# Kernel tuning notes

Hardware: AMD Instinct MI355X
Metric: run time of the kernel (lower is better)

## Reference

```python
import jax, jax.numpy as jnp
import numpy as np

B, T, DIM, LDIM, NAUX = 4096, 64, 16, 64, 32
H, AH = 256, 128
DT = 0.01
N_SHIFTS = 64
EPS = 1e-5


def _bn(x, g, b):
    # BatchNorm1d in training mode: batch stats, biased variance
    m = jnp.mean(x, 0)
    v = jnp.mean((x - m) ** 2, 0)
    return (x - m) / jnp.sqrt(v + EPS) * g + b


def _forward(xs, enc_bn_gamma, enc_bn_beta, enc_W1, enc_b1, enc_W2, enc_b2, enc_W3,
             enc_scale, aux_bn_gamma, aux_bn_beta, aux_W1, aux_b1, aux_W2, aux_b2,
             aux_W3, aux_scale, Cw):
    lrelu = jax.nn.leaky_relu  # negative_slope=0.01, matches F.leaky_relu default

    # ---- aux nets: 32 small MLPs on x0, vectorized over net index k ----
    x0 = xs[:, 0, :]                                   # [B, DIM]
    m = jnp.mean(x0, 0)
    v = jnp.mean((x0 - m) ** 2, 0)
    xn = (x0 - m) / jnp.sqrt(v + EPS)                  # shared batch stats
    xa = xn[None] * aux_bn_gamma[:, None, :] + aux_bn_beta[:, None, :]  # [K,B,DIM]
    h = lrelu(jnp.einsum('kbi,kji->kbj', xa, aux_W1) + aux_b1[:, None, :])
    h = lrelu(jnp.einsum('kbi,kji->kbj', h, aux_W2) + aux_b2[:, None, :])
    aux = (jnp.einsum('kbi,kji->kbj', h, aux_W3) * aux_scale[:, None, :])
    aux = aux.transpose(1, 0, 2)                       # [B, NAUX, 2] = (mu, omega)

    scale = jnp.exp(aux[..., 0] * DT)                  # [B, NAUX]
    cost = jnp.cos(aux[..., 1] * DT) * scale
    sint = jnp.sin(aux[..., 1] * DT) * scale

    # ---- encoder over trajectory ----
    xs_t = xs[:, :N_SHIFTS, :]                         # [B, T, DIM]
    xf = _bn(xs_t.reshape(-1, DIM), enc_bn_gamma, enc_bn_beta)
    hf = lrelu(xf @ enc_W1.T + enc_b1)
    hf = lrelu(hf @ enc_W2.T + enc_b2)
    yenc = ((hf @ enc_W3.T) * enc_scale).reshape(B, N_SHIFTS, LDIM)
    y = jnp.concatenate((xs_t, yenc), -1)              # [B, T, DIM+LDIM]

    # ---- Jordan-block Koopman recurrence: y @ blockdiag([[c,s],[-s,c]]) ----
    y0 = yenc[:, 0]                                    # [B, LDIM]

    def step(yc, _):
        yb = yc.reshape(B, NAUX, 2)
        o0 = cost * yb[..., 0] - sint * yb[..., 1]
        o1 = sint * yb[..., 0] + cost * yb[..., 1]
        yn = jnp.stack((o0, o1), -1).reshape(B, LDIM)
        return yn, (yn @ Cw.T, yn)

    _, (xseq, yseq) = jax.lax.scan(step, y0, None, length=N_SHIFTS - 1)
    x_pred = jnp.concatenate((xs_t[:, :1], xseq.transpose(1, 0, 2)), 1)   # [B,T,DIM]
    yl_pred = jnp.concatenate((y0[:, None], yseq.transpose(1, 0, 2)), 1)  # [B,T,LDIM]
    y_pred = jnp.concatenate((x_pred, yl_pred), -1)
    return y, y_pred


def setup_inputs() -> dict:
    key = jax.random.key(0)
    ks = jax.random.split(key, 10)
    r = lambda k, s, sc: jax.random.normal(k, s, jnp.float32) * sc
    return {
        'xs': jax.random.normal(ks[0], (B, T, DIM), jnp.float32),
        'enc_bn_gamma': jnp.ones((DIM,), jnp.float32),
        'enc_bn_beta': jnp.zeros((DIM,), jnp.float32),
        'enc_W1': r(ks[1], (H, DIM), 0.2),
        'enc_b1': jnp.zeros((H,), jnp.float32),
        'enc_W2': r(ks[2], (H, H), 0.06),
        'enc_b2': jnp.zeros((H,), jnp.float32),
        'enc_W3': r(ks[3], (LDIM, H), 0.06),
        'enc_scale': jnp.ones((LDIM,), jnp.float32),
        'aux_bn_gamma': jnp.ones((NAUX, DIM), jnp.float32),
        'aux_bn_beta': jnp.zeros((NAUX, DIM), jnp.float32),
        'aux_W1': r(ks[4], (NAUX, AH, DIM), 0.2),
        'aux_b1': jnp.zeros((NAUX, AH), jnp.float32),
        'aux_W2': r(ks[5], (NAUX, AH, AH), 0.09),
        'aux_b2': jnp.zeros((NAUX, AH), jnp.float32),
        'aux_W3': r(ks[6], (NAUX, 2, AH), 0.09),
        'aux_scale': jnp.ones((NAUX, 2), jnp.float32),
        'Cw': r(ks[7], (DIM, LDIM), 0.1),
    }


def reference(xs, enc_bn_gamma, enc_bn_beta, enc_W1, enc_b1, enc_W2, enc_b2, enc_W3,
              enc_scale, aux_bn_gamma, aux_bn_beta, aux_W1, aux_b1, aux_W2, aux_b2,
              aux_W3, aux_scale, Cw):
    return _forward(xs, enc_bn_gamma, enc_bn_beta, enc_W1, enc_b1, enc_W2, enc_b2,
                    enc_W3, enc_scale, aux_bn_gamma, aux_bn_beta, aux_W1, aux_b1,
                    aux_W2, aux_b2, aux_W3, aux_scale, Cw)
```

## Files before the change

### kernel.cpp

```cpp
#include <hip/hip_runtime.h>
#include <cstddef>

#define NBATCH 4096
#define NTIME  64
#define NDIM   16
#define NLDIM  64
#define NAUXK  32
#define NAH    128
#define NH     256
#define MROWS  (NBATCH*NTIME)
#define DT_C   0.01f
#define EPS_C  1e-5f
#define ENC_ITER 2
#define ENC_BLOCKS (MROWS/(64*ENC_ITER))
#define AUX_BLOCKS (NAUXK*64)
#define ESTR 264
#define ASTR 136

using short8 = __attribute__((ext_vector_type(8))) short;
using short4v = __attribute__((ext_vector_type(4))) short;
using f32x4 = __attribute__((ext_vector_type(4))) float;

__device__ __forceinline__ float lrelu(float x){ return fmaxf(x, 0.01f*x); }
__device__ __forceinline__ unsigned short f2bf(float f){
    unsigned u = __builtin_bit_cast(unsigned, f);
    u += 0x7fff + ((u>>16)&1u);
    return (unsigned short)(u>>16);
}
__device__ __forceinline__ unsigned cvt_pk(float a, float b){
    unsigned r;
    asm("v_cvt_pk_bf16_f32 %0, %1, %2" : "=v"(r) : "v"(a), "v"(b));
    return r;
}
__device__ __forceinline__ short4v pack4(f32x4 a){
    uint2 u;
    u.x = cvt_pk(lrelu(a[0]), lrelu(a[1]));
    u.y = cvt_pk(lrelu(a[2]), lrelu(a[3]));
    return __builtin_bit_cast(short4v, u);
}

template<int STRIDE>
__device__ __forceinline__ short8 ld_h(const unsigned short* hb, int m, int c){
    return *(const short8*)&hb[m*STRIDE + c];
}
template<int STRIDE>
__device__ __forceinline__ void st_h(unsigned short* hb, int m, int c, short4v p){
    *(short4v*)&hb[m*STRIDE + c] = p;
}

__global__ __launch_bounds__(256) void k_mega1(const float* __restrict__ W1,
                                               const float* __restrict__ W2,
                                               const float* __restrict__ W3,
                                               const float* __restrict__ ag,
                                               const float* __restrict__ aW1,
                                               const float* __restrict__ aW2,
                                               const float* __restrict__ aW3,
                                               const float* __restrict__ ab1,
                                               const float* __restrict__ abt,
                                               const float* __restrict__ xs,
                                               unsigned short* __restrict__ dst,
                                               float* __restrict__ b1p,
                                               float* __restrict__ part,
                                               float* __restrict__ part2){
    __shared__ float red[256*33];
    const int blk = blockIdx.x;
    const int tid = threadIdx.x;

    if(blk < 2896){
        int i = blk*256 + tid;
        float v;
        if(i < 4096){ v = W1[i]; }
        else if(i < 69632){
            int e = i - 4096;
            int kt = e>>13, r = e&8191;
            int rb = r>>9, sft = r&511;
            int l = sft>>3, j = sft&7;
            int g = l>>4, arw = l&15;
            v = W2[(rb*16+arw)*256 + kt*32 + g*8 + j];
        } else if(i < 86016){
            int e = i - 69632;
            int kt = e>>11, r = e&2047;
            int rb = r>>9, sft = r&511;
            int l = sft>>3, j = sft&7;
            int g = l>>4, arw = l&15;
            v = W3[(rb*16+arw)*256 + kt*32 + g*8 + j];
        } else if(i < 151552){
            int e = i - 86016; int k = e>>11, n = (e>>4)&127, c = e&15;
            v = aW1[(k*128+n)*16 + c] * ag[k*16+c];
        } else if(i < 675840){
            int e = i - 151552; int k = e>>14, kt = (e>>12)&3, n = (e>>5)&127, j = e&31;
            v = aW2[(k*128+n)*128 + kt*32 + j];
        } else if(i < 741376){
            int e = i - 675840; int k = e>>11, kt = (e>>9)&3, n = (e>>5)&15, j = e&31;
            v = (n < 2) ? aW3[(k*2+n)*128 + kt*32 + j] : 0.f;
        } else return;
        dst[i] = f2bf(v);
    } else if(blk < 2912){
        int i = (blk-2896)*256 + tid;
        int k = i>>7, n = i&127;
        const float* wr = aW1 + (size_t)(k*128+n)*16;
        const float* bt = abt + k*16;
        float a = ab1[i];
#pragma unroll
        for(int c=0;c<16;c++) a += wr[c]*bt[c];
        b1p[i] = a;
    } else if(blk < 3168){
        int sblk = blk - 2912;
        float s[16], q[16];
#pragma unroll
        for(int i=0;i<16;i++){ s[i]=0.f; q[i]=0.f; }
        int r0 = sblk*(MROWS/256) + tid;
        for(int j=0;j<4;j++){
            const float4* p = (const float4*)(xs + (size_t)(r0 + j*256)*NDIM);
#pragma unroll
            for(int v=0; v<4; v++){
                float4 f = p[v];
                s[v*4+0]+=f.x; q[v*4+0]+=f.x*f.x;
                s[v*4+1]+=f.y; q[v*4+1]+=f.y*f.y;
                s[v*4+2]+=f.z; q[v*4+2]+=f.z*f.z;
                s[v*4+3]+=f.w; q[v*4+3]+=f.w*f.w;
            }
        }
#pragma unroll
        for(int i=0;i<16;i++){ red[tid*33+i]=s[i]; red[tid*33+16+i]=q[i]; }
        __syncthreads();
        for(int off=128; off>0; off>>=1){
            if(tid < off){
#pragma unroll
                for(int i=0;i<32;i++) red[tid*33+i] += red[(tid+off)*33+i];
            }
            __syncthreads();
        }
        if(tid < 32) part[sblk*32 + tid] = red[tid];
    } else {
        int sblk = blk - 3168;
        int b = sblk*256 + tid;
        const float4* p = (const float4*)(xs + (size_t)b*(NTIME*NDIM));
#pragma unroll
        for(int v=0; v<4; v++){
            float4 f = p[v];
            red[tid*33 + v*4+0] = f.x; red[tid*33+16 + v*4+0] = f.x*f.x;
            red[tid*33 + v*4+1] = f.y; red[tid*33+16 + v*4+1] = f.y*f.y;
            red[tid*33 + v*4+2] = f.z; red[tid*33+16 + v*4+2] = f.z*f.z;
            red[tid*33 + v*4+3] = f.w; red[tid*33+16 + v*4+3] = f.w*f.w;
        }
        __syncthreads();
        for(int off=128; off>0; off>>=1){
            if(tid < off){
#pragma unroll
                for(int i=0;i<32;i++) red[tid*33+i] += red[(tid+off)*33+i];
            }
            __syncthreads();
        }
        if(tid < 32) part2[sblk*32 + tid] = red[tid];
    }
}

__global__ __launch_bounds__(256) void k_finalize(const float* __restrict__ part,
                                                  const float* __restrict__ part2,
                                                  const float* __restrict__ gamma,
                                                  const float* __restrict__ beta,
                                                  float* __restrict__ stats){
    __shared__ float red[256*33];
    __shared__ float x0tot[32];
    int tid = threadIdx.x;
#pragma unroll
    for(int i=0;i<32;i++) red[tid*33+i] = (tid < 16) ? part2[tid*32+i] : 0.f;
    __syncthreads();
    for(int off=8; off>0; off>>=1){
        if(tid < off){
#pragma unroll
            for(int i=0;i<32;i++) red[tid*33+i] += red[(tid+off)*33+i];
        }
        __syncthreads();
    }
    if(tid < 32) x0tot[tid] = red[tid];
    __syncthreads();
#pragma unroll
    for(int i=0;i<32;i++) red[tid*33+i] = part[tid*32+i];
    __syncthreads();
    for(int off=128; off>0; off>>=1){
        if(tid < off){
#pragma unroll
            for(int i=0;i<32;i++) red[tid*33+i] += red[(tid+off)*33+i];
        }
        __syncthreads();
    }
    if(tid < 16){
        int i = tid;
        float m0 = x0tot[i] / (float)NBATCH;
        float v0 = x0tot[16+i] / (float)NBATCH - m0*m0;
        stats[32+i] = m0;
        stats[48+i] = 1.0f / sqrtf(v0 + EPS_C);
        float me = red[i] / (float)MROWS;
        float ve = red[16+i] / (float)MROWS - me*me;
        float a = gamma[i] / sqrtf(ve + EPS_C);
        stats[i]      = a;
        stats[16+i]   = beta[i] - me*a;
    }
}

__device__ __forceinline__ void enc_body(unsigned short* smem, int eb, int tid,
                                         const float* __restrict__ xs,
                                         const float* __restrict__ stats,
                                         const unsigned short* __restrict__ W1bf,
                                         const float* __restrict__ b1,
                                         const unsigned short* __restrict__ W2s,
                                         const float* __restrict__ b2,
                                         const unsigned short* __restrict__ W3s,
                                         const float* __restrict__ esc,
                                         float* __restrict__ outy){
    unsigned short* xa = smem;
    unsigned short* hb = smem + 1024;

    const int w    = tid >> 6;
    const int lane = tid & 63;
    const int g    = lane >> 4;
    const int arow = lane & 15;
    const int mh   = w & 1;
    const int nt3  = w >> 1;

    const int c2  = (tid & 7)*2;
    const int r0p = tid >> 3;
    const float sa0 = stats[c2],    sa1 = stats[c2+1];
    const float sb0 = stats[16+c2], sb1 = stats[16+c2+1];

    const unsigned short* w2base = W2s + (w*2)*512 + lane*8;
    const unsigned short* w3base = W3s + nt3*512 + lane*8;

    for(int it=0; it<ENC_ITER; it++){
        const int m0 = (eb*ENC_ITER + it)*64;

        short8 wcur[2];
        wcur[0] = *(const short8*)&w2base[0];
        wcur[1] = *(const short8*)&w2base[512];

        {
            float2 v = *(const float2*)(xs + (size_t)(m0 + r0p)*NDIM + c2);
            *(float2*)(outy + (size_t)(m0 + r0p)*80 + c2) = v;
            unsigned u = cvt_pk(v.x*sa0 + sb0, v.y*sa1 + sb1);
            *(unsigned*)&xa[r0p*16 + c2] = u;
        }
        __syncthreads();

#pragma unroll
        for(int nt=0; nt<2; nt++){
            short8 aw = {0,0,0,0,0,0,0,0};
            if(lane < 32) aw = *(const short8*)&W1bf[(w*32 + nt*16 + arow)*16 + g*8];
            float4 b4 = *(const float4*)&b1[w*32 + nt*16 + g*4];
            f32x4 bi = {b4.x, b4.y, b4.z, b4.w};
#pragma unroll
            for(int mt=0; mt<4; mt++){
                short8 bx = {0,0,0,0,0,0,0,0};
                if(lane < 32) bx = *(const short8*)&xa[(mt*16 + arow)*16 + g*8];
                f32x4 a = __builtin_amdgcn_mfma_f32_16x16x32_bf16(aw, bx, bi, 0, 0, 0);
                st_h<ESTR>(hb, mt*16 + arow, w*32 + nt*16 + g*4, pack4(a));
            }
        }
        __syncthreads();

        f32x4 acc[2][4];
#pragma unroll
        for(int nt=0; nt<2; nt++){
            float4 b4 = *(const float4*)&b2[w*32 + nt*16 + g*4];
            f32x4 bi = {b4.x, b4.y, b4.z, b4.w};
#pragma unroll
            for(int m=0;m<4;m++) acc[nt][m] = bi;
        }

#pragma unroll 1
        for(int kt=0; kt<8; kt++){
            short8 wn0={0,0,0,0,0,0,0,0}, wn1=wn0;
            if(kt < 7){
                const unsigned short* wp = w2base + (kt+1)*8192;
                wn0 = *(const short8*)&wp[0];
                wn1 = *(const short8*)&wp[512];
            }
#pragma unroll
            for(int mt=0; mt<4; mt++){
                short8 bh = ld_h<ESTR>(hb, mt*16 + arow, kt*32 + g*8);
                acc[0][mt] = __builtin_amdgcn_mfma_f32_16x16x32_bf16(wcur[0], bh, acc[0][mt], 0, 0, 0);
                acc[1][mt] = __builtin_amdgcn_mfma_f32_16x16x32_bf16(wcur[1], bh, acc[1][mt], 0, 0, 0);
            }
            wcur[0]=wn0; wcur[1]=wn1;
        }
        __syncthreads();

#pragma unroll
        for(int nt=0; nt<2; nt++)
#pragma unroll
            for(int mt=0; mt<4; mt++)
                st_h<ESTR>(hb, mt*16 + arow, w*32 + nt*16 + g*4, pack4(acc[nt][mt]));
        __syncthreads();

        f32x4 acc3[2];
        acc3[0] = (f32x4){0.f,0.f,0.f,0.f};
        acc3[1] = (f32x4){0.f,0.f,0.f,0.f};
#pragma unroll 1
        for(int kt=0; kt<8; kt++){
            short8 aw3 = *(const short8*)&w3base[kt*2048];
#pragma unroll
            for(int i=0;i<2;i++){
                int mt = mh*2 + i;
                short8 bh = ld_h<ESTR>(hb, mt*16 + arow, kt*32 + g*8);
                acc3[i] = __builtin_amdgcn_mfma_f32_16x16x32_bf16(aw3, bh, acc3[i], 0, 0, 0);
            }
        }

        {
            int nc = nt3*16 + g*4;
            float4 e4 = *(const float4*)&esc[nc];
#pragma unroll
            for(int i=0;i<2;i++){
                int mt = mh*2 + i;
                float4 o;
                o.x = acc3[i][0]*e4.x;
                o.y = acc3[i][1]*e4.y;
                o.z = acc3[i][2]*e4.z;
                o.w = acc3[i][3]*e4.w;
                *(float4*)&outy[(size_t)(m0 + mt*16 + arow)*80 + 16 + nc] = o;
            }
        }
        if(it+1 < ENC_ITER) __syncthreads();
    }
}

__device__ __forceinline__ void aux_body(unsigned short* smem, int ab, int tid,
                                         const float* __restrict__ xs,
                                         const float* __restrict__ stats,
                                         const unsigned short* __restrict__ W1s,
                                         const float* __restrict__ b1p,
                                         const unsigned short* __restrict__ W2s,
                                         const float* __restrict__ ab2,
                                         const unsigned short* __restrict__ W3s,
                                         const float* __restrict__ asc,
                                         float* __restrict__ auxout){
    unsigned short* xa = smem;
    unsigned short* hb = smem + 1024;

    const int w    = tid >> 6;
    const int lane = tid & 63;
    const int g    = lane >> 4;
    const int arow = lane & 15;
    const int k    = ab >> 6;
    const int b0   = (ab & 63) * 64;

    short8 w1r = {0,0,0,0,0,0,0,0};
    if(lane < 32) w1r = *(const short8*)&W1s[(size_t)k*2048 + (w*16 + arow)*16 + g*8];
    short8 w2r[4];
#pragma unroll
    for(int kt=0; kt<4; kt++)
        w2r[kt] = *(const short8*)&W2s[(size_t)k*16384 + kt*4096 + (w*16 + arow)*32 + g*8];
    short8 w3r[4];
#pragma unroll
    for(int kt=0; kt<4; kt++)
        w3r[kt] = *(const short8*)&W3s[(size_t)k*2048 + kt*512 + arow*32 + g*8];

    {
        const int c2  = (tid & 7)*2;
        const int r0p = tid >> 3;
        float2 v = *(const float2*)(xs + (size_t)(b0 + r0p)*(NTIME*NDIM) + c2);
        unsigned u = cvt_pk((v.x - stats[32+c2])*stats[48+c2],
                            (v.y - stats[32+c2+1])*stats[48+c2+1]);
        *(unsigned*)&xa[r0p*16 + c2] = u;
    }
    __syncthreads();

    {
        float4 b4 = *(const float4*)&b1p[k*128 + w*16 + g*4];
        f32x4 bi = {b4.x, b4.y, b4.z, b4.w};
#pragma unroll
        for(int mt=0; mt<4; mt++){
            short8 bx = {0,0,0,0,0,0,0,0};
            if(lane < 32) bx = *(const short8*)&xa[(mt*16 + arow)*16 + g*8];
            f32x4 a = __builtin_amdgcn_mfma_f32_16x16x32_bf16(w1r, bx, bi, 0, 0, 0);
            st_h<ASTR>(hb, mt*16 + arow, w*16 + g*4, pack4(a));
        }
    }
    __syncthreads();

    f32x4 acc2[4];
    {
        float4 b4 = *(const float4*)&ab2[k*128 + w*16 + g*4];
        f32x4 bi = {b4.x, b4.y, b4.z, b4.w};
#pragma unroll
        for(int m=0;m<4;m++) acc2[m] = bi;
    }
#pragma unroll
    for(int kt=0; kt<4; kt++){
#pragma unroll
        for(int mt=0; mt<4; mt++){
            short8 bh = ld_h<ASTR>(hb, mt*16 + arow, kt*32 + g*8);
            acc2[mt] = __builtin_amdgcn_mfma_f32_16x16x32_bf16(w2r[kt], bh, acc2[mt], 0, 0, 0);
        }
    }
    __syncthreads();

#pragma unroll
    for(int mt=0; mt<4; mt++)
        st_h<ASTR>(hb, mt*16 + arow, w*16 + g*4, pack4(acc2[mt]));
    __syncthreads();

    if(w < 4){
        f32x4 acc3 = {0.f,0.f,0.f,0.f};
#pragma unroll
        for(int kt=0; kt<4; kt++){
            short8 bh = ld_h<ASTR>(hb, w*16 + arow, kt*32 + g*8);
            acc3 = __builtin_amdgcn_mfma_f32_16x16x32_bf16(w3r[kt], bh, acc3, 0, 0, 0);
        }
        if(g == 0){
            float2 o;
            o.x = acc3[0] * asc[k*2+0] * DT_C;
            o.y = acc3[1] * asc[k*2+1] * DT_C;
            *(float2*)&auxout[(size_t)(b0 + w*16 + arow)*64 + 2*k] = o;
        }
    }
}

__global__ __launch_bounds__(512) void k_mega2(const float* __restrict__ xs,
                                               const float* __restrict__ stats,
                                               const unsigned short* __restrict__ W1bf,
                                               const float* __restrict__ b1,
                                               const unsigned short* __restrict__ W2s,
                                               const float* __restrict__ b2,
                                               const unsigned short* __restrict__ W3s,
                                               const float* __restrict__ esc,
                                               const unsigned short* __restrict__ aW1s,
                                               const float* __restrict__ b1p,
                                               const unsigned short* __restrict__ aW2s,
                                               const float* __restrict__ ab2,
                                               const unsigned short* __restrict__ aW3s,
                                               const float* __restrict__ asc,
                                               float* __restrict__ outy,
                                               float* __restrict__ auxout){
    __shared__ unsigned short smem[1024 + 64*ESTR];
    const int blk = blockIdx.x;
    const int tid = threadIdx.x;
    if(blk < ENC_BLOCKS){
        enc_body(smem, blk, tid, xs, stats, W1bf, b1, W2s, b2, W3s, esc, outy);
    } else {
        aux_body(smem, blk - ENC_BLOCKS, tid, xs, stats, aW1s, b1p, aW2s, ab2, aW3s, asc, auxout);
    }
}

__global__ __launch_bounds__(256) void k_pred(const float* __restrict__ xs,
                                              const float* __restrict__ auxbuf,
                                              const float* __restrict__ Cw,
                                              const float* __restrict__ outy,
                                              float* __restrict__ outyp){
    __shared__ float cw[16*64];
    const int tid = threadIdx.x;
    for(int j=tid; j<1024; j+=256) cw[j] = Cw[j];
    __syncthreads();

    int gid = blockIdx.x*256 + tid;
    int b = gid >> 6;
    int t = gid & 63;
    const float* yb = outy + (size_t)b*(NTIME*80) + 16;
    const float* ab = auxbuf + (size_t)b*64;
    float tt = (float)t;

    float y[64];
#pragma unroll
    for(int k=0;k<32;k++){
        float th0 = ab[2*k+0];
        float th1 = ab[2*k+1];
        float scl = __expf(th0*tt);
        float cc  = __cosf(th1*tt)*scl;
        float ss  = __sinf(th1*tt)*scl;
        float2 y01 = *(const float2*)&yb[2*k];
        y[2*k+0] = cc*y01.x - ss*y01.y;
        y[2*k+1] = ss*y01.x + cc*y01.y;
    }

    float* orow = outyp + (size_t)(b*NTIME + t)*80;
    if(t == 0){
        const float4* p = (const float4*)(xs + (size_t)b*(NTIME*NDIM));
#pragma unroll
        for(int i4=0;i4<4;i4++) *(float4*)&orow[i4*4] = p[i4];
    } else {
#pragma unroll
        for(int i4=0;i4<4;i4++){
            float o[4];
#pragma unroll
            for(int ii=0;ii<4;ii++){
                int i = i4*4+ii;
                float a = 0.f;
#pragma unroll
                for(int j4=0;j4<16;j4++){
                    float4 c4 = *(const float4*)&cw[i*64 + j4*4];
                    a += c4.x*y[j4*4+0] + c4.y*y[j4*4+1] + c4.z*y[j4*4+2] + c4.w*y[j4*4+3];
                }
                o[ii] = a;
            }
            *(float4*)&orow[i4*4] = make_float4(o[0],o[1],o[2],o[3]);
        }
    }
#pragma unroll
    for(int j4=0;j4<16;j4++){
        *(float4*)&orow[16+j4*4] = make_float4(y[j4*4+0],y[j4*4+1],y[j4*4+2],y[j4*4+3]);
    }
}

extern "C" void kernel_launch(void* const* d_in, const int* in_sizes, int n_in,
                              void* d_out, int out_size, void* d_ws, size_t ws_size,
                              hipStream_t stream) {
    const float* xs     = (const float*)d_in[0];
    const float* enc_g  = (const float*)d_in[1];
    const float* enc_bt = (const float*)d_in[2];
    const float* eW1    = (const float*)d_in[3];
    const float* eb1    = (const float*)d_in[4];
    const float* eW2    = (const float*)d_in[5];
    const float* eb2    = (const float*)d_in[6];
    const float* eW3    = (const float*)d_in[7];
    const float* esc    = (const float*)d_in[8];
    const float* ag     = (const float*)d_in[9];
    const float* abt    = (const float*)d_in[10];
    const float* aW1    = (const float*)d_in[11];
    const float* ab1    = (const float*)d_in[12];
    const float* aW2    = (const float*)d_in[13];
    const float* ab2    = (const float*)d_in[14];
    const float* aW3    = (const float*)d_in[15];
    const float* asc    = (const float*)d_in[16];
    const float* Cw     = (const float*)d_in[17];

    float* out   = (float*)d_out;
    float* ws    = (float*)d_ws;
    float* part   = ws;
    float* stats  = ws + 8192;
    float* part2  = ws + 8256;
    float* auxout = ws + 8768;
    float* b1p    = ws + 270912;
    unsigned short* wbf = (unsigned short*)(ws + 275008);
    unsigned short* W1bf = wbf;
    unsigned short* W2s  = wbf + 4096;
    unsigned short* W3s  = wbf + 69632;
    unsigned short* aW1s = wbf + 86016;
    unsigned short* aW2s = wbf + 151552;
    unsigned short* aW3s = wbf + 675840;

    float* outy  = out;
    float* outyp = out + (size_t)NBATCH*NTIME*80;

    k_mega1<<<3184, 256, 0, stream>>>(eW1, eW2, eW3, ag, aW1, aW2, aW3,
                                      ab1, abt, xs, wbf, b1p, part, part2);
    k_finalize<<<1, 256, 0, stream>>>(part, part2, enc_g, enc_bt, stats);
    k_mega2<<<ENC_BLOCKS + AUX_BLOCKS, 512, 0, stream>>>(
        xs, stats, W1bf, eb1, W2s, eb2, W3s, esc,
        aW1s, b1p, aW2s, ab2, aW3s, asc, outy, auxout);
    k_pred<<<MROWS/256, 256, 0, stream>>>(xs, auxout, Cw, outy, outyp);
}
```

Measured before the change: 138.8 us.

## Fold output scales into bf16 weights, widen stats partials, restructure W2 prefetch

Folds the encoder scale and the aux scale times DT into the bf16-converted W3 weights during preprocessing, so the epilogues no longer multiply by them. The statistics pass now uses four times as many blocks, each reducing a single row per thread, and the finalize kernel sums four partials per thread. The encoder W2 MFMA loop is unrolled by two with explicit A/B register double-buffering of weight fragments. Together these aim to raise parallelism in the stats reduction and hide weight-load latency, at the cost of more workspace and extra bf16 rounding applied to the scaled weights.

```diff
diff --git a/kernel.cpp b/kernel.cpp
--- a/kernel.cpp
+++ b/kernel.cpp
@@ -51,10 +51,12 @@
 __global__ __launch_bounds__(256) void k_mega1(const float* __restrict__ W1,
                                                const float* __restrict__ W2,
                                                const float* __restrict__ W3,
+                                               const float* __restrict__ esc,
                                                const float* __restrict__ ag,
                                                const float* __restrict__ aW1,
                                                const float* __restrict__ aW2,
                                                const float* __restrict__ aW3,
+                                               const float* __restrict__ asc,
                                                const float* __restrict__ ab1,
                                                const float* __restrict__ abt,
                                                const float* __restrict__ xs,
@@ -83,7 +85,8 @@
             int rb = r>>9, sft = r&511;
             int l = sft>>3, j = sft&7;
             int g = l>>4, arw = l&15;
-            v = W3[(rb*16+arw)*256 + kt*32 + g*8 + j];
+            int n = rb*16 + arw;
+            v = W3[n*256 + kt*32 + g*8 + j] * esc[n];
         } else if(i < 151552){
             int e = i - 86016; int k = e>>11, n = (e>>4)&127, c = e&15;
             v = aW1[(k*128+n)*16 + c] * ag[k*16+c];
@@ -92,7 +95,7 @@
             v = aW2[(k*128+n)*128 + kt*32 + j];
         } else if(i < 741376){
             int e = i - 675840; int k = e>>11, kt = (e>>9)&3, n = (e>>5)&15, j = e&31;
-            v = (n < 2) ? aW3[(k*2+n)*128 + kt*32 + j] : 0.f;
+            v = (n < 2) ? aW3[(k*2+n)*128 + kt*32 + j] * asc[k*2+n] * DT_C : 0.f;
         } else return;
         dst[i] = f2bf(v);
     } else if(blk < 2912){
@@ -104,22 +107,18 @@
 #pragma unroll
         for(int c=0;c<16;c++) a += wr[c]*bt[c];
         b1p[i] = a;
-    } else if(blk < 3168){
+    } else if(blk < 3936){
         int sblk = blk - 2912;
+        int r0 = sblk*256 + tid;
+        const float4* p = (const float4*)(xs + (size_t)r0*NDIM);
         float s[16], q[16];
 #pragma unroll
-        for(int i=0;i<16;i++){ s[i]=0.f; q[i]=0.f; }
-        int r0 = sblk*(MROWS/256) + tid;
-        for(int j=0;j<4;j++){
-            const float4* p = (const float4*)(xs + (size_t)(r0 + j*256)*NDIM);
-#pragma unroll
-            for(int v=0; v<4; v++){
-                float4 f = p[v];
-                s[v*4+0]+=f.x; q[v*4+0]+=f.x*f.x;
-                s[v*4+1]+=f.y; q[v*4+1]+=f.y*f.y;
-                s[v*4+2]+=f.z; q[v*4+2]+=f.z*f.z;
-                s[v*4+3]+=f.w; q[v*4+3]+=f.w*f.w;
-            }
+        for(int v=0; v<4; v++){
+            float4 f = p[v];
+            s[v*4+0]=f.x; q[v*4+0]=f.x*f.x;
+            s[v*4+1]=f.y; q[v*4+1]=f.y*f.y;
+            s[v*4+2]=f.z; q[v*4+2]=f.z*f.z;
+            s[v*4+3]=f.w; q[v*4+3]=f.w*f.w;
         }
 #pragma unroll
         for(int i=0;i<16;i++){ red[tid*33+i]=s[i]; red[tid*33+16+i]=q[i]; }
@@ -133,7 +132,7 @@
         }
         if(tid < 32) part[sblk*32 + tid] = red[tid];
     } else {
-        int sblk = blk - 3168;
+        int sblk = blk - 3936;
         int b = sblk*256 + tid;
         const float4* p = (const float4*)(xs + (size_t)b*(NTIME*NDIM));
 #pragma unroll
@@ -177,7 +176,11 @@
     if(tid < 32) x0tot[tid] = red[tid];
     __syncthreads();
 #pragma unroll
-    for(int i=0;i<32;i++) red[tid*33+i] = part[tid*32+i];
+    for(int i=0;i<32;i++){
+        float a = part[tid*32+i] + part[(tid+256)*32+i]
+                + part[(tid+512)*32+i] + part[(tid+768)*32+i];
+        red[tid*33+i] = a;
+    }
     __syncthreads();
     for(int off=128; off>0; off>>=1){
         if(tid < off){
@@ -208,7 +211,6 @@
                                          const unsigned short* __restrict__ W2s,
                                          const float* __restrict__ b2,
                                          const unsigned short* __restrict__ W3s,
-                                         const float* __restrict__ esc,
                                          float* __restrict__ outy){
     unsigned short* xa = smem;
     unsigned short* hb = smem + 1024;
@@ -231,9 +233,8 @@
     for(int it=0; it<ENC_ITER; it++){
         const int m0 = (eb*ENC_ITER + it)*64;
 
-        short8 wcur[2];
-        wcur[0] = *(const short8*)&w2base[0];
-        wcur[1] = *(const short8*)&w2base[512];
+        short8 bA0 = *(const short8*)&w2base[0];
+        short8 bA1 = *(const short8*)&w2base[512];
 
         {
             float2 v = *(const float2*)(xs + (size_t)(m0 + r0p)*NDIM + c2);
@@ -269,20 +270,28 @@
         }
 
 #pragma unroll 1
-        for(int kt=0; kt<8; kt++){
-            short8 wn0={0,0,0,0,0,0,0,0}, wn1=wn0;
-            if(kt < 7){
-                const unsigned short* wp = w2base + (kt+1)*8192;
-                wn0 = *(const short8*)&wp[0];
-                wn1 = *(const short8*)&wp[512];
-            }
+        for(int i2=0; i2<4; i2++){
+            const int kt0 = i2*2, kt1 = i2*2+1;
+            const unsigned short* wp1 = w2base + kt1*8192;
+            short8 bB0 = *(const short8*)&wp1[0];
+            short8 bB1 = *(const short8*)&wp1[512];
 #pragma unroll
             for(int mt=0; mt<4; mt++){
-                short8 bh = ld_h<ESTR>(hb, mt*16 + arow, kt*32 + g*8);
-                acc[0][mt] = __builtin_amdgcn_mfma_f32_16x16x32_bf16(wcur[0], bh, acc[0][mt], 0, 0, 0);
-                acc[1][mt] = __builtin_amdgcn_mfma_f32_16x16x32_bf16(wcur[1], bh, acc[1][mt], 0, 0, 0);
-            }
-            wcur[0]=wn0; wcur[1]=wn1;
+                short8 bh = ld_h<ESTR>(hb, mt*16 + arow, kt0*32 + g*8);
+                acc[0][mt] = __builtin_amdgcn_mfma_f32_16x16x32_bf16(bA0, bh, acc[0][mt], 0, 0, 0);
+                acc[1][mt] = __builtin_amdgcn_mfma_f32_16x16x32_bf16(bA1, bh, acc[1][mt], 0, 0, 0);
+            }
+            if(i2 < 3){
+                const unsigned short* wp2 = w2base + (kt0+2)*8192;
+                bA0 = *(const short8*)&wp2[0];
+                bA1 = *(const short8*)&wp2[512];
+            }
+#pragma unroll
+            for(int mt=0; mt<4; mt++){
+                short8 bh = ld_h<ESTR>(hb, mt*16 + arow, kt1*32 + g*8);
+                acc[0][mt] = __builtin_amdgcn_mfma_f32_16x16x32_bf16(bB0, bh, acc[0][mt], 0, 0, 0);
+                acc[1][mt] = __builtin_amdgcn_mfma_f32_16x16x32_bf16(bB1, bh, acc[1][mt], 0, 0, 0);
+            }
         }
         __syncthreads();
 
@@ -309,15 +318,14 @@
 
         {
             int nc = nt3*16 + g*4;
-            float4 e4 = *(const float4*)&esc[nc];
 #pragma unroll
             for(int i=0;i<2;i++){
                 int mt = mh*2 + i;
                 float4 o;
-                o.x = acc3[i][0]*e4.x;
-                o.y = acc3[i][1]*e4.y;
-                o.z = acc3[i][2]*e4.z;
-                o.w = acc3[i][3]*e4.w;
+                o.x = acc3[i][0];
+                o.y = acc3[i][1];
+                o.z = acc3[i][2];
+                o.w = acc3[i][3];
                 *(float4*)&outy[(size_t)(m0 + mt*16 + arow)*80 + 16 + nc] = o;
             }
         }
@@ -333,7 +341,6 @@
                                          const unsigned short* __restrict__ W2s,
                                          const float* __restrict__ ab2,
                                          const unsigned short* __restrict__ W3s,
-                                         const float* __restrict__ asc,
                                          float* __restrict__ auxout){
     unsigned short* xa = smem;
     unsigned short* hb = smem + 1024;
@@ -410,8 +417,8 @@
         }
         if(g == 0){
             float2 o;
-            o.x = acc3[0] * asc[k*2+0] * DT_C;
-            o.y = acc3[1] * asc[k*2+1] * DT_C;
+            o.x = acc3[0];
+            o.y = acc3[1];
             *(float2*)&auxout[(size_t)(b0 + w*16 + arow)*64 + 2*k] = o;
         }
     }
@@ -424,22 +431,20 @@
                                                const unsigned short* __restrict__ W2s,
                                                const float* __restrict__ b2,
                                                const unsigned short* __restrict__ W3s,
-                                               const float* __restrict__ esc,
                                                const unsigned short* __restrict__ aW1s,
                                                const float* __restrict__ b1p,
                                                const unsigned short* __restrict__ aW2s,
                                                const float* __restrict__ ab2,
                                                const unsigned short* __restrict__ aW3s,
-                                               const float* __restrict__ asc,
                                                float* __restrict__ outy,
                                                float* __restrict__ auxout){
     __shared__ unsigned short smem[1024 + 64*ESTR];
     const int blk = blockIdx.x;
     const int tid = threadIdx.x;
     if(blk < ENC_BLOCKS){
-        enc_body(smem, blk, tid, xs, stats, W1bf, b1, W2s, b2, W3s, esc, outy);
+        enc_body(smem, blk, tid, xs, stats, W1bf, b1, W2s, b2, W3s, outy);
     } else {
-        aux_body(smem, blk - ENC_BLOCKS, tid, xs, stats, aW1s, b1p, aW2s, ab2, aW3s, asc, auxout);
+        aux_body(smem, blk - ENC_BLOCKS, tid, xs, stats, aW1s, b1p, aW2s, ab2, aW3s, auxout);
     }
 }
 
@@ -527,11 +532,11 @@
     float* out   = (float*)d_out;
     float* ws    = (float*)d_ws;
     float* part   = ws;
-    float* stats  = ws + 8192;
-    float* part2  = ws + 8256;
-    float* auxout = ws + 8768;
-    float* b1p    = ws + 270912;
-    unsigned short* wbf = (unsigned short*)(ws + 275008);
+    float* stats  = ws + 32768;
+    float* part2  = ws + 32832;
+    float* auxout = ws + 33344;
+    float* b1p    = ws + 295488;
+    unsigned short* wbf = (unsigned short*)(ws + 299584);
     unsigned short* W1bf = wbf;
     unsigned short* W2s  = wbf + 4096;
     unsigned short* W3s  = wbf + 69632;
@@ -542,11 +547,11 @@
     float* outy  = out;
     float* outyp = out + (size_t)NBATCH*NTIME*80;
 
-    k_mega1<<<3184, 256, 0, stream>>>(eW1, eW2, eW3, ag, aW1, aW2, aW3,
+    k_mega1<<<3952, 256, 0, stream>>>(eW1, eW2, eW3, esc, ag, aW1, aW2, aW3, asc,
                                       ab1, abt, xs, wbf, b1p, part, part2);
     k_finalize<<<1, 256, 0, stream>>>(part, part2, enc_g, enc_bt, stats);
     k_mega2<<<ENC_BLOCKS + AUX_BLOCKS, 512, 0, stream>>>(
-        xs, stats, W1bf, eb1, W2s, eb2, W3s, esc,
-        aW1s, b1p, aW2s, ab2, aW3s, asc, outy, auxout);
+        xs, stats, W1bf, eb1, W2s, eb2, W3s,
+        aW1s, b1p, aW2s, ab2, aW3s, outy, auxout);
     k_pred<<<MROWS/256, 256, 0, stream>>>(xs, auxout, Cw, outy, outyp);
 }
```

Result: no change. 139.7 us (+0.6%).
